# Kernel optimization log

Hardware: AMD Instinct MI355X
Metric: run time of the kernel (lower is better)

Reference implementation:

```python
import jax, jax.numpy as jnp
import numpy as np

PRED_STEPS = 5
NEG = 16
C = 256
B = 64
H = 16
W = 16
SKIP = 1
EPS = 1e-11


def setup_inputs() -> dict:
    key = jax.random.key(0)
    ks = jax.random.split(key, 3 + PRED_STEPS)
    inp = {
        "z": jax.random.normal(ks[0], (B, C, H, W), jnp.float32),
        "c": jax.random.normal(ks[1], (B, C, H, W), jnp.float32),
        "Wk": jax.random.normal(ks[2], (PRED_STEPS, C, C), jnp.float32) * 0.05,
    }
    for k in range(1, PRED_STEPS + 1):
        rows = (H - k - SKIP) * W * B
        inp[f"rand_idx_{k}"] = jax.random.randint(ks[2 + k], (rows * NEG,), 0, rows, dtype=jnp.int64 if jax.config.jax_enable_x64 else jnp.int32)
    return inp


def reference(z, c, Wk, rand_idx_1, rand_idx_2, rand_idx_3, rand_idx_4, rand_idx_5):
    idx_list = [rand_idx_1, rand_idx_2, rand_idx_3, rand_idx_4, rand_idx_5]
    total_loss = jnp.float32(0.0)
    patchwise_loss = jnp.zeros((B, H, W), jnp.float32)
    patchwise_count = jnp.zeros((H, W), jnp.float32)
    for k in range(1, PRED_STEPS + 1):
        off = k + SKIP
        Hk = H - off
        # 1x1 conv projection, permuted to [Hk, W, B, C]
        ztwk = jnp.einsum('oi,bihw->hwbo', Wk[k - 1], z[:, :, off:, :])
        # random-gather negatives: [Hk, W, B, NEG, C]
        flat = ztwk.reshape(Hk * W * B, C)
        ztwk_shuf = flat[idx_list[k - 1]].reshape(Hk, W, B, NEG, C)
        # context: [Hk, W, B, C]
        ctx = jnp.transpose(c[:, :, :Hk, :], (2, 3, 0, 1))
        # scoring
        main = jnp.einsum('hwbc,hwbc->hwb', ctx, ztwk)[..., None]        # [Hk,W,B,1]
        negs = jnp.einsum('hwbc,hwbnc->hwbn', ctx, ztwk_shuf)            # [Hk,W,B,NEG]
        logits = jnp.concatenate([main, negs], axis=-1)                  # [Hk,W,B,1+NEG]
        log_fk = jnp.transpose(logits, (2, 3, 0, 1))                     # [B,1+NEG,Hk,W]
        sm = jax.nn.softmax(log_fk, axis=1)
        stu_loss = -jnp.log(sm[:, 0, :, :] + EPS)                        # [B,Hk,W]
        total_loss = total_loss + stu_loss.mean()
        patchwise_loss = patchwise_loss.at[:, off:, :].add(stu_loss)
        patchwise_loss = patchwise_loss.at[:, :H - off, :].add(stu_loss)
        ones = jnp.ones((Hk, W), jnp.float32)
        patchwise_count = patchwise_count.at[off:, :].add(ones)
        patchwise_count = patchwise_count.at[:H - off, :].add(ones)
    total_loss = total_loss / PRED_STEPS
    return (total_loss, patchwise_loss, patchwise_count)
```

## Files before the change

kernel.cpp:

```cpp
#include <hip/hip_runtime.h>
#include <hip/hip_bf16.h>
#include <math.h>

#define NEG_ 16
#define PRED_ 5
#define EPS_ 1e-11f
#define LDW 18
#define GSTR 272
#define ASTR 72

typedef __attribute__((ext_vector_type(8))) short bf16x8;
typedef __attribute__((ext_vector_type(4))) float f32x4;

static __device__ __forceinline__ unsigned short f2bu(float f) {
  __hip_bfloat16 h = __float2bfloat16(f);
  return *(unsigned short*)&h;
}


__global__ __launch_bounds__(256) void prep_all(
    const float* __restrict__ z, const float* __restrict__ c,
    const float* __restrict__ Wk,
    unsigned short* __restrict__ Zp, unsigned short* __restrict__ Cb,
    unsigned short* __restrict__ Wb) {
  __shared__ float tile[32][65];
  const int t = threadIdx.x;
  if (blockIdx.y == 7) {
    int ib = blockIdx.z * 256 + blockIdx.x;
    if (ib < 320) {
      int i = ib * 256 + t;
      float4 v = ((const float4*)Wk)[i];
      ushort4 o;
      o.x = f2bu(v.x); o.y = f2bu(v.y); o.z = f2bu(v.z); o.w = f2bu(v.w);
      ((ushort4*)Wb)[i] = o;
    }
    return;
  }
  const float* in = blockIdx.z ? c : z;
  unsigned short* out = blockIdx.z ? Cb : Zp;
  const int p0 = blockIdx.x * 64;
  const int q0 = blockIdx.y * 32 + (blockIdx.z ? 0 : 32);
  const int tx = t & 31, ty = t >> 5;
#pragma unroll
  for (int r = 0; r < 64; r += 8)
    tile[tx][ty + r] = in[(size_t)(p0 + ty + r) * 256 + q0 + tx];
  __syncthreads();
  const int pp = t & 63, wq = t >> 6;
#pragma unroll
  for (int r = 0; r < 32; r += 4)
    out[(size_t)(q0 + wq + r) * 16384 + p0 + pp] = f2bu(tile[wq + r][pp]);
}

__global__ __launch_bounds__(256) void gemm_all(
    const unsigned short* __restrict__ Zp, const unsigned short* __restrict__ Wb,
    unsigned short* __restrict__ Yb) {
  const int kk = blockIdx.z;
  const int Mk = (14 - kk) * 1024;
  const int m0b = blockIdx.y * 128;
  if (m0b >= Mk) return;
  const unsigned short* A = Zp + (size_t)(kk + 2) * 1024 * 256;
  const unsigned short* Wm = Wb + (size_t)kk * 65536;
  unsigned short* Y = Yb + (size_t)kk * 14336 * 256;
  __shared__ unsigned short As[128 * ASTR];
  __shared__ unsigned short Bs[128 * ASTR];
  const int t = threadIdx.x;
  const int wid = t >> 6, lane = t & 63;
  const int wm = wid >> 1, wn = wid & 1;
  const int l15 = lane & 15, quad = lane >> 4;
  const int n0 = blockIdx.x * 128;
  const int srow = t >> 1, shalf = t & 1;
  const unsigned short* ga = A + (size_t)(m0b + srow) * 256 + shalf * 32;
  const unsigned short* gb = Wm + (size_t)(n0 + srow) * 256 + shalf * 32;
  unsigned short* wa = As + srow * ASTR + shalf * 32;
  unsigned short* wb = Bs + srow * ASTR + shalf * 32;
  f32x4 acc[4][4] = {};
  bf16x8 ra[4], rb[4];
#pragma unroll
  for (int cs = 0; cs < 4; ++cs) {
    ra[cs] = *(const bf16x8*)(ga + cs * 8);
    rb[cs] = *(const bf16x8*)(gb + cs * 8);
  }
#pragma unroll
  for (int ki = 0; ki < 4; ++ki) {
    __syncthreads();
#pragma unroll
    for (int cs = 0; cs < 4; ++cs) {
      *(bf16x8*)(wa + cs * 8) = ra[cs];
      *(bf16x8*)(wb + cs * 8) = rb[cs];
    }
    __syncthreads();
    if (ki < 3) {
      const int k1 = (ki + 1) * 64;
#pragma unroll
      for (int cs = 0; cs < 4; ++cs) {
        ra[cs] = *(const bf16x8*)(ga + k1 + cs * 8);
        rb[cs] = *(const bf16x8*)(gb + k1 + cs * 8);
      }
    }
#pragma unroll
    for (int ks = 0; ks < 2; ++ks) {
      bf16x8 af[4], bf[4];
#pragma unroll
      for (int tm = 0; tm < 4; ++tm)
        af[tm] = *(const bf16x8*)(As + (wm * 64 + tm * 16 + l15) * ASTR + ks * 32 + quad * 8);
#pragma unroll
      for (int tn = 0; tn < 4; ++tn)
        bf[tn] = *(const bf16x8*)(Bs + (wn * 64 + tn * 16 + l15) * ASTR + ks * 32 + quad * 8);
#pragma unroll
      for (int tm = 0; tm < 4; ++tm)
#pragma unroll
        for (int tn = 0; tn < 4; ++tn)
          acc[tm][tn] = __builtin_amdgcn_mfma_f32_16x16x32_bf16(
              af[tm], bf[tn], acc[tm][tn], 0, 0, 0);
    }
  }
#pragma unroll
  for (int tm = 0; tm < 4; ++tm)
#pragma unroll
    for (int tn = 0; tn < 4; ++tn)
#pragma unroll
      for (int r = 0; r < 4; ++r)
        Y[(size_t)(m0b + wm * 64 + tm * 16 + quad * 4 + r) * 256 +
          n0 + wn * 64 + tn * 16 + l15] = f2bu(acc[tm][tn][r]);
}

__global__ __launch_bounds__(256) void score_all(
    const unsigned short* __restrict__ Yb, const unsigned short* __restrict__ Cb,
    const int* __restrict__ r1, const int* __restrict__ r2,
    const int* __restrict__ r3, const int* __restrict__ r4,
    const int* __restrict__ r5, float* __restrict__ Lk) {
  __shared__ __align__(16) unsigned short gbuf[4][16 * GSTR];
  __shared__ float L[16 * LDW];
  const int wv = threadIdx.x >> 6, lane = threadIdx.x & 63;
  const int gid = blockIdx.x;
  int kk, base;
  if (gid < 896)       { kk = 0; base = 0; }
  else if (gid < 1728) { kk = 1; base = 896; }
  else if (gid < 2496) { kk = 2; base = 1728; }
  else if (gid < 3200) { kk = 3; base = 2496; }
  else                 { kk = 4; base = 3200; }
  const int Mk = (14 - kk) * 1024;
  const int m0 = (gid - base) * 16;
  const int* ridx = kk == 0 ? r1 : kk == 1 ? r2 : kk == 2 ? r3 : kk == 3 ? r4 : r5;
  const unsigned short* Y = Yb + (size_t)kk * 14336 * 256;
  const int l15 = lane & 15, quad = lane >> 4;
  const int half = lane >> 5, ch = lane & 31;
  unsigned short* mybuf = gbuf[wv];

  auto gather = [&](const unsigned short* src, int iv, bf16x8* dst) {
#pragma unroll
    for (int j = 0; j < 8; ++j) {
      int rlo = __shfl(iv, 2 * j);
      int rhi = __shfl(iv, 2 * j + 1);
      int row = half ? rhi : rlo;
      dst[j] = *(const bf16x8*)(src + (size_t)row * 256 + ch * 8);
    }
  };
  auto stage = [&](const bf16x8* g) {
#pragma unroll
    for (int j2 = 0; j2 < 8; ++j2)
      *(bf16x8*)(mybuf + (2 * j2 + half) * GSTR + ch * 8) = g[j2];
  };

  const int c0 = (wv == 0) ? 0 : (4 * wv + 1);
  const int nc = (wv == 0) ? 5 : 4;
  int iv[5];
#pragma unroll
  for (int j = 0; j < 5; ++j) {
    if (j < nc) {
      const int c = c0 + j;
      if (c == 0) iv[j] = m0 + l15;
      else {
        int idx = ridx[(m0 + (c - 1)) * NEG_ + l15];
        iv[j] = idx < 0 ? 0 : (idx >= Mk ? Mk - 1 : idx);
      }
    } else iv[j] = 0;
  }

  bf16x8 af[8];
  {
    bf16x8 g[8];
    gather(Cb, m0 + l15, g);
    stage(g);
#pragma unroll
    for (int tv = 0; tv < 8; ++tv)
      af[tv] = *(const bf16x8*)(mybuf + l15 * GSTR + quad * 8 + tv * 32);
  }

  bf16x8 g[8], gn[8];
  gather(Y, iv[0], g);
  for (int j = 0; j < nc; ++j) {
    if (j + 1 < nc) gather(Y, iv[j + 1], gn);
    stage(g);
    f32x4 acc = {};
#pragma unroll
    for (int tv = 0; tv < 8; ++tv) {
      bf16x8 bf = *(const bf16x8*)(mybuf + l15 * GSTR + quad * 8 + tv * 32);
      acc = __builtin_amdgcn_mfma_f32_16x16x32_bf16(af[tv], bf, acc, 0, 0, 0);
    }
    const int c = c0 + j;
    if (c == 0) {
#pragma unroll
      for (int r = 0; r < 4; ++r)
        if (l15 == quad * 4 + r) L[(quad * 4 + r) * LDW] = acc[r];
    } else {
      const int i = c - 1;
      if (quad == (i >> 2)) L[i * LDW + 1 + l15] = acc[i & 3];
    }
#pragma unroll
    for (int tv = 0; tv < 8; ++tv) g[tv] = gn[tv];
  }
  __syncthreads();
  if (threadIdx.x < 16) {
    float mainv = L[threadIdx.x * LDW];
    float mx = mainv;
    float nv[NEG_];
#pragma unroll
    for (int n = 0; n < NEG_; ++n) {
      nv[n] = L[threadIdx.x * LDW + 1 + n];
      mx = fmaxf(mx, nv[n]);
    }
    float num = __expf(mainv - mx);
    float se = num;
#pragma unroll
    for (int n = 0; n < NEG_; ++n) se += __expf(nv[n] - mx);
    Lk[kk * 14336 + m0 + threadIdx.x] = -logf(num / se + EPS_);
  }
}

__global__ __launch_bounds__(256) void finalize_pl(
    const float* __restrict__ Lk, float* __restrict__ out) {
  if (blockIdx.x < 64) {
    int idx = blockIdx.x * 256 + threadIdx.x;
    int b = idx >> 8, h = (idx >> 4) & 15, w = idx & 15;
    float v = 0.f;
#pragma unroll
    for (int kk = 0; kk < PRED_; ++kk) {
      int off = kk + 2;
      if (h >= off)      v += Lk[kk * 14336 + ((h - off) * 16 + w) * 64 + b];
      if (h <= 15 - off) v += Lk[kk * 14336 + (h * 16 + w) * 64 + b];
    }
    out[1 + idx] = v;
    if (idx < 256) {
      int hh = idx >> 4;
      float cnt = 0.f;
#pragma unroll
      for (int off = 2; off <= 6; ++off)
        cnt += (hh >= off ? 1.f : 0.f) + (hh <= 15 - off ? 1.f : 0.f);
      out[1 + 16384 + idx] = cnt;
    }
  } else {
    __shared__ float red[256];
    const int t = threadIdx.x;
    float local = 0.f;
#pragma unroll
    for (int kk = 0; kk < PRED_; ++kk) {
      const int Mk = (14 - kk) * 1024;
      const float scale = 1.0f / (5120.0f * (float)(14 - kk));
      for (int e = t; e < Mk; e += 256)
        local += Lk[kk * 14336 + e] * scale;
    }
    red[t] = local;
    __syncthreads();
    for (int s = 128; s; s >>= 1) {
      if (t < s) red[t] += red[t + s];
      __syncthreads();
    }
    if (t == 0) out[0] = red[0];
  }
}

extern "C" void kernel_launch(void* const* d_in, const int* in_sizes, int n_in,
                              void* d_out, int out_size, void* d_ws, size_t ws_size,
                              hipStream_t stream) {
  const float* z  = (const float*)d_in[0];
  const float* c  = (const float*)d_in[1];
  const float* Wk = (const float*)d_in[2];
  float* out = (float*)d_out;
  char* wsb = (char*)d_ws;
  unsigned short* Zp = (unsigned short*)(wsb);
  unsigned short* Cb = (unsigned short*)(wsb + 8388608);
  unsigned short* Wb = (unsigned short*)(wsb + 16777216);
  unsigned short* Yb = (unsigned short*)(wsb + 17432576);
  float*          Lk = (float*)(wsb + 54132736);

  prep_all<<<dim3(256, 8, 2), 256, 0, stream>>>(z, c, Wk, Zp, Cb, Wb);
  gemm_all<<<dim3(2, 112, PRED_), 256, 0, stream>>>(Zp, Wb, Yb);
  score_all<<<3840, 256, 0, stream>>>(
      Yb, Cb, (const int*)d_in[3], (const int*)d_in[4], (const int*)d_in[5],
      (const int*)d_in[6], (const int*)d_in[7], Lk);
  finalize_pl<<<65, 256, 0, stream>>>(Lk, out);
}
```

Measured before the change: 181.4 us.

## Project context with transposed Wk instead of projecting z before gathering

Uses the identity ctx·(W z) = (Wᵀ ctx)·z. The GEMM now projects the bf16 context rows with a transposed Wk, and the scoring kernel gathers raw bf16 z rows for both the positive and the negative samples. Random gathers then read from the shared 8 MB Zp buffer rather than five separate projected-z buffers, and every GEMM step reads the same A matrix, which should improve L2 locality. In exchange, prep gains a tiled transpose of Wk through shared memory.

Result: faster. 174.6 us (-3.7%).

```diff
diff --git a/kernel.cpp b/kernel.cpp
--- a/kernel.cpp
+++ b/kernel.cpp
@@ -28,11 +28,16 @@
   if (blockIdx.y == 7) {
     int ib = blockIdx.z * 256 + blockIdx.x;
     if (ib < 320) {
-      int i = ib * 256 + t;
-      float4 v = ((const float4*)Wk)[i];
-      ushort4 o;
-      o.x = f2bu(v.x); o.y = f2bu(v.y); o.z = f2bu(v.z); o.w = f2bu(v.w);
-      ((ushort4*)Wb)[i] = o;
+      const int k = ib >> 6, tl = ib & 63;
+      const int r0 = (tl >> 3) * 32, c0g = (tl & 7) * 32;
+      const int tx = t & 31, ty = t >> 5;
+#pragma unroll
+      for (int r = 0; r < 32; r += 8)
+        tile[ty + r][tx] = Wk[k * 65536 + (r0 + ty + r) * 256 + c0g + tx];
+      __syncthreads();
+#pragma unroll
+      for (int r = 0; r < 32; r += 8)
+        Wb[k * 65536 + (c0g + ty + r) * 256 + r0 + tx] = f2bu(tile[tx][ty + r]);
     }
     return;
   }
@@ -52,15 +57,15 @@
 }
 
 __global__ __launch_bounds__(256) void gemm_all(
-    const unsigned short* __restrict__ Zp, const unsigned short* __restrict__ Wb,
-    unsigned short* __restrict__ Yb) {
+    const unsigned short* __restrict__ Cb, const unsigned short* __restrict__ Wb,
+    unsigned short* __restrict__ Cw) {
   const int kk = blockIdx.z;
   const int Mk = (14 - kk) * 1024;
   const int m0b = blockIdx.y * 128;
   if (m0b >= Mk) return;
-  const unsigned short* A = Zp + (size_t)(kk + 2) * 1024 * 256;
+  const unsigned short* A = Cb;
   const unsigned short* Wm = Wb + (size_t)kk * 65536;
-  unsigned short* Y = Yb + (size_t)kk * 14336 * 256;
+  unsigned short* Y = Cw + (size_t)kk * 14336 * 256;
   __shared__ unsigned short As[128 * ASTR];
   __shared__ unsigned short Bs[128 * ASTR];
   const int t = threadIdx.x;
@@ -125,7 +130,7 @@
 }
 
 __global__ __launch_bounds__(256) void score_all(
-    const unsigned short* __restrict__ Yb, const unsigned short* __restrict__ Cb,
+    const unsigned short* __restrict__ Cw, const unsigned short* __restrict__ Zp,
     const int* __restrict__ r1, const int* __restrict__ r2,
     const int* __restrict__ r3, const int* __restrict__ r4,
     const int* __restrict__ r5, float* __restrict__ Lk) {
@@ -142,7 +147,8 @@
   const int Mk = (14 - kk) * 1024;
   const int m0 = (gid - base) * 16;
   const int* ridx = kk == 0 ? r1 : kk == 1 ? r2 : kk == 2 ? r3 : kk == 3 ? r4 : r5;
-  const unsigned short* Y = Yb + (size_t)kk * 14336 * 256;
+  const unsigned short* Yc = Cw + (size_t)kk * 14336 * 256;
+  const unsigned short* Z  = Zp + (size_t)(kk + 2) * 1024 * 256;
   const int l15 = lane & 15, quad = lane >> 4;
   const int half = lane >> 5, ch = lane & 31;
   unsigned short* mybuf = gbuf[wv];
@@ -180,7 +186,7 @@
   bf16x8 af[8];
   {
     bf16x8 g[8];
-    gather(Cb, m0 + l15, g);
+    gather(Yc, m0 + l15, g);
     stage(g);
 #pragma unroll
     for (int tv = 0; tv < 8; ++tv)
@@ -188,9 +194,9 @@
   }
 
   bf16x8 g[8], gn[8];
-  gather(Y, iv[0], g);
+  gather(Z, iv[0], g);
   for (int j = 0; j < nc; ++j) {
-    if (j + 1 < nc) gather(Y, iv[j + 1], gn);
+    if (j + 1 < nc) gather(Z, iv[j + 1], gn);
     stage(g);
     f32x4 acc = {};
 #pragma unroll
@@ -281,13 +287,13 @@
   unsigned short* Zp = (unsigned short*)(wsb);
   unsigned short* Cb = (unsigned short*)(wsb + 8388608);
   unsigned short* Wb = (unsigned short*)(wsb + 16777216);
-  unsigned short* Yb = (unsigned short*)(wsb + 17432576);
+  unsigned short* Cw = (unsigned short*)(wsb + 17432576);
   float*          Lk = (float*)(wsb + 54132736);
 
   prep_all<<<dim3(256, 8, 2), 256, 0, stream>>>(z, c, Wk, Zp, Cb, Wb);
-  gemm_all<<<dim3(2, 112, PRED_), 256, 0, stream>>>(Zp, Wb, Yb);
+  gemm_all<<<dim3(2, 112, PRED_), 256, 0, stream>>>(Cb, Wb, Cw);
   score_all<<<3840, 256, 0, stream>>>(
-      Yb, Cb, (const int*)d_in[3], (const int*)d_in[4], (const int*)d_in[5],
+      Cw, Zp, (const int*)d_in[3], (const int*)d_in[4], (const int*)d_in[5],
       (const int*)d_in[6], (const int*)d_in[7], Lk);
   finalize_pl<<<65, 256, 0, stream>>>(Lk, out);
 }
```
